# Performance work log

Measured on AMD Instinct MI355X. Metric: run time of the kernel, lower is better.

The kernel has to match this reference:

```python
import jax, jax.numpy as jnp
import numpy as np

D_MODEL = 2048
H_Q = 16
H_KV = 4
D_HEAD = D_MODEL // H_Q  # 128
G = H_Q // H_KV          # 4
B, S = 4, 2048


def setup_inputs() -> dict:
    key = jax.random.key(0)
    k1, k2, k3 = jax.random.split(key, 3)
    x = jax.random.normal(k1, (B, S, D_MODEL), dtype=jnp.float32)
    mask = jnp.zeros((S, S), dtype=jnp.float32)  # additive mask (zeros == no masking)
    # Linear weights, torch layout [out_features, in_features], bias=False
    Wqkv = jax.random.normal(k2, ((H_Q + 2 * H_KV) * D_HEAD, D_MODEL), dtype=jnp.float32) * (1.0 / np.sqrt(D_MODEL))
    Wo = jax.random.normal(k3, (D_MODEL, D_MODEL), dtype=jnp.float32) * (1.0 / np.sqrt(D_MODEL))
    return {"x": x, "mask": mask, "Wqkv": Wqkv, "Wo": Wo}


def reference(x, mask, Wqkv, Wo):
    d_q = H_Q * D_HEAD
    d_kv = H_KV * D_HEAD
    # fused QKV projection (Linear, no bias): x @ Wqkv.T
    qkv = jnp.einsum('bsd,ed->bse', x, Wqkv)  # [B,S,(H_Q+2*H_KV)*D_HEAD]
    q, k, v = jnp.split(qkv, [d_q, d_q + d_kv], axis=-1)
    q = q.reshape(B, S, H_Q, D_HEAD)
    k = k.reshape(B, S, H_KV, D_HEAD)
    v = v.reshape(B, S, H_KV, D_HEAD)
    # GQA: repeat_interleave KV heads G times along head axis
    k = jnp.repeat(k, G, axis=-2)  # [B,S,H_Q,D_HEAD]
    v = jnp.repeat(v, G, axis=-2)
    scale = 1.0 / np.sqrt(D_HEAD).astype(np.float32)
    scores = jnp.einsum('bqhd,bkhd->bhqk', q, k) * scale + mask  # [B,H_Q,S,S]
    attn = jax.nn.softmax(scores, axis=-1)
    out = jnp.einsum('bhqk,bkhd->bqhd', attn, v)  # [B,S,H_Q,D_HEAD]
    out = out.reshape(B, S, D_MODEL)
    return jnp.einsum('bsd,ed->bse', out, Wo)  # output projection
```

## Files before the change

kernel.cpp:

```cpp
#include <hip/hip_runtime.h>

#define D_MODEL 2048
#define S_LEN 2048
#define HQ 16
#define HKV 4
#define DH 128
#define QKV_W 3072
#define M_TOK 8192

typedef unsigned short u16;
typedef __bf16 bf16x8 __attribute__((ext_vector_type(8)));
typedef float f32x4 __attribute__((ext_vector_type(4)));
typedef float f32x16 __attribute__((ext_vector_type(16)));

__device__ __forceinline__ u16 f2bf(float f) {
  union { float f; unsigned u; } v; v.f = f;
  unsigned u = v.u;
  return (u16)((u + 0x7fffu + ((u >> 16) & 1u)) >> 16);
}

__device__ __forceinline__ bf16x8 ld_frag(const u16* p) {
  bf16x8 r; __builtin_memcpy(&r, p, 16); return r;
}

__device__ __forceinline__ void gl_lds16(const u16* g, u16* l) {
  __builtin_amdgcn_global_load_lds(
      (const __attribute__((address_space(1))) void*)g,
      (__attribute__((address_space(3))) void*)l, 16, 0, 0);
}

__device__ __forceinline__ unsigned cvtpk(float lo, float hi_) {
  unsigned r;
  asm("v_cvt_pk_bf16_f32 %0, %1, %2" : "=v"(r) : "v"(lo), "v"(hi_));
  return r;
}

#define MFMA(a, b, c) __builtin_amdgcn_mfma_f32_16x16x32_bf16(a, b, c, 0, 0, 0)
#define MFMA32(a, b, c) __builtin_amdgcn_mfma_f32_32x32x16_bf16(a, b, c, 0, 0, 0)

__device__ __forceinline__ float vmax16(const f32x16& v) {
  float a = fmaxf(fmaxf(v[0], v[1]), fmaxf(v[2], v[3]));
  float b = fmaxf(fmaxf(v[4], v[5]), fmaxf(v[6], v[7]));
  float c = fmaxf(fmaxf(v[8], v[9]), fmaxf(v[10], v[11]));
  float d = fmaxf(fmaxf(v[12], v[13]), fmaxf(v[14], v[15]));
  return fmaxf(fmaxf(a, b), fmaxf(c, d));
}
__device__ __forceinline__ float vsum16(const f32x16& v) {
  float a = (v[0] + v[1]) + (v[2] + v[3]);
  float b = (v[4] + v[5]) + (v[6] + v[7]);
  float c = (v[8] + v[9]) + (v[10] + v[11]);
  float d = (v[12] + v[13]) + (v[14] + v[15]);
  return (a + b) + (c + d);
}

__global__ __launch_bounds__(256) void k_f32_to_bf16(const float* __restrict__ s,
                                                     u16* __restrict__ d,
                                                     long scale_n) {
  long i = (long)(blockIdx.x * 256 + threadIdx.x) * 8;
  float sc = (i < scale_n) ? 0.08838834764831845f : 1.0f;
  float a[8];
  __builtin_memcpy(a, s + i, 32);
  u16 r[8];
#pragma unroll
  for (int j = 0; j < 8; ++j) r[j] = f2bf(a[j] * sc);
  __builtin_memcpy(d + i, r, 16);
}

template <int OUT_BF16>
__global__ __launch_bounds__(512, 2) void k_gemm256(const u16* __restrict__ A,
                                                    const u16* __restrict__ B,
                                                    void* __restrict__ C,
                                                    int M, int N, int K) {
  __shared__ u16 As[2][16384];
  __shared__ u16 Bs[2][16384];
  const int tid = threadIdx.x;
  const int lane = tid & 63;
  const int wid = tid >> 6;
  const int l15 = lane & 15, l4 = lane >> 4;
  const int wr = wid >> 2, wc = wid & 3;

  const int swz = (blockIdx.x & 7) * (gridDim.x >> 3) + (blockIdx.x >> 3);
  const int mt = M >> 8;
  const long tm = (long)(swz % mt) * 256;
  const long tn = (long)(swz / mt) * 256;

  const int cA = l4 ^ ((l15 >> 1) & 3);
  const int arow = wr * 128 + l15;
  const int brow = wc * 64 + l15;

  f32x4 acc[8][4] = {};
  bf16x8 af[4], bfr[4];

#define STG(dst, src, tbase, s, koff)                                      \
  do {                                                                     \
    _Pragma("unroll") for (int j = 0; j < 2; ++j) {                        \
      int p = tid + j * 512;                                               \
      int row = p >> 2, cc = p & 3;                                        \
      int g = cc ^ ((row >> 1) & 3);                                       \
      gl_lds16(src + (tbase + row) * (long)K + (koff) + (s) * 32 + g * 8,  \
               (dst) + (s) * 8192 + p * 8);                                \
    }                                                                      \
  } while (0)

#define DSR_A(ptr, s, mh)                                                  \
  _Pragma("unroll") for (int m = 0; m < 4; ++m)                            \
      af[m] = ld_frag((ptr) + (s) * 8192 + (arow + (mh) * 64 + m * 16) * 32 + cA * 8);
#define DSR_B(ptr, s)                                                      \
  _Pragma("unroll") for (int n = 0; n < 4; ++n)                            \
      bfr[n] = ld_frag((ptr) + (s) * 8192 + (brow + n * 16) * 32 + cA * 8);
#define MM(mh)                                                             \
  _Pragma("unroll") for (int m = 0; m < 4; ++m)                            \
      _Pragma("unroll") for (int n = 0; n < 4; ++n)                        \
          acc[(mh) * 4 + m][n] = MFMA(af[m], bfr[n], acc[(mh) * 4 + m][n]);
#define LGKM0                                              \
  asm volatile("s_waitcnt lgkmcnt(0)" ::: "memory");       \
  __builtin_amdgcn_sched_barrier(0)

  const int NT = K >> 6;
  STG(&As[0][0], A, tm, 0, 0);
  STG(&Bs[0][0], B, tn, 0, 0);
  STG(&As[0][0], A, tm, 1, 0);
  STG(&Bs[0][0], B, tn, 1, 0);

  for (int t = 0; t < NT; ++t) {
    const u16* as_ = &As[t & 1][0];
    const u16* bs_ = &Bs[t & 1][0];
    u16* an_ = &As[(t + 1) & 1][0];
    u16* bn_ = &Bs[(t + 1) & 1][0];
    const long kn = (long)(t + 1) * 64;
    const bool st = (t + 1 < NT);

    asm volatile("s_waitcnt vmcnt(4)" ::: "memory");
    __builtin_amdgcn_s_barrier();
    DSR_A(as_, 0, 0);
    DSR_B(bs_, 0);
    if (st) STG(an_, A, tm, 0, kn);
    LGKM0;
    __builtin_amdgcn_s_setprio(1); MM(0); __builtin_amdgcn_s_setprio(0);

    __builtin_amdgcn_s_barrier();
    DSR_A(as_, 0, 1);
    if (st) STG(bn_, B, tn, 0, kn);
    LGKM0;
    __builtin_amdgcn_s_setprio(1); MM(1); __builtin_amdgcn_s_setprio(0);

    if (st) {
      asm volatile("s_waitcnt vmcnt(4)" ::: "memory");
    } else {
      asm volatile("s_waitcnt vmcnt(0)" ::: "memory");
    }
    __builtin_amdgcn_s_barrier();
    DSR_A(as_, 1, 0);
    DSR_B(bs_, 1);
    if (st) STG(an_, A, tm, 1, kn);
    LGKM0;
    __builtin_amdgcn_s_setprio(1); MM(0); __builtin_amdgcn_s_setprio(0);

    __builtin_amdgcn_s_barrier();
    DSR_A(as_, 1, 1);
    if (st) STG(bn_, B, tn, 1, kn);
    LGKM0;
    __builtin_amdgcn_s_setprio(1); MM(1); __builtin_amdgcn_s_setprio(0);
  }
#undef STG
#undef DSR_A
#undef DSR_B
#undef MM
#undef LGKM0

#pragma unroll
  for (int m = 0; m < 8; ++m)
#pragma unroll
    for (int n = 0; n < 4; ++n)
#pragma unroll
      for (int i = 0; i < 4; ++i) {
        long row = tm + wr * 128 + m * 16 + l4 * 4 + i;
        long col = tn + wc * 64 + n * 16 + l15;
        if (OUT_BF16)
          ((u16*)C)[row * N + col] = f2bf(acc[m][n][i]);
        else
          ((float*)C)[row * N + col] = acc[m][n][i];
      }
}

__global__ __launch_bounds__(256) void k_vtrans(const u16* __restrict__ qkv,
                                                u16* __restrict__ vt) {
  __shared__ u16 T[64][68];
  const int tid = threadIdx.x;
  const int st = blockIdx.x;
  const int dt = blockIdx.y;
  const int bh = blockIdx.z;
  const int b = bh >> 2, kvh = bh & 3;
  const long s0 = (long)st * 64, d0 = (long)dt * 64;
#pragma unroll
  for (int j = 0; j < 2; ++j) {
    int chunk = tid + j * 256;
    int row = chunk >> 3, c8 = chunk & 7;
    u16 tmp[8];
    __builtin_memcpy(tmp,
                     qkv + ((long)b * S_LEN + s0 + row) * QKV_W + 2560 +
                         kvh * DH + d0 + c8 * 8,
                     16);
    __builtin_memcpy(&T[row][c8 * 8], tmp, 16);
  }
  __syncthreads();
#pragma unroll
  for (int j = 0; j < 2; ++j) {
    int chunk = tid + j * 256;
    int drow = chunk >> 3, c8 = chunk & 7;
    u16 tmp[8];
#pragma unroll
    for (int e = 0; e < 8; ++e) tmp[e] = T[c8 * 8 + e][drow];
    __builtin_memcpy(vt + ((long)bh * DH + d0 + drow) * S_LEN + s0 + c8 * 8,
                     tmp, 16);
  }
}

__global__ __launch_bounds__(512, 2) void k_attn(const u16* __restrict__ qkv,
                                                 const u16* __restrict__ vt,
                                                 u16* __restrict__ ao) {
  __shared__ u16 Ks[2][64 * 128];
  __shared__ u16 Vs[2][128 * 64];
  const int tid = threadIdx.x;
  const int lane = tid & 63;
  const int wid = tid >> 6;
  const int l31 = lane & 31, hi = lane >> 5;
  const int qt = blockIdx.x & 7;
  const int hh = (blockIdx.x >> 3) & 3;
  const int bkv = blockIdx.x >> 5;
  const int b = bkv >> 2, kvh = bkv & 3;
  const int h = kvh * 4 + hh;
  const long rowbase = (long)b * S_LEN;
  const int q0 = qt * 256 + wid * 32;
  const long vbase = (long)bkv * DH * S_LEN;

  bf16x8 qf[8];
  {
    const u16* qrow = qkv + (rowbase + q0 + l31) * QKV_W + h * DH;
#pragma unroll
    for (int kk = 0; kk < 8; ++kk) qf[kk] = ld_frag(qrow + kk * 16 + hi * 8);
  }

  f32x16 o[4] = {};
  float m_run = -3.0e38f, l_run = 0.f;

#define STAGE(buf, tile)                                                      \
  do {                                                                        \
    long s0_ = (long)(tile) * 64;                                             \
    _Pragma("unroll") for (int j = 0; j < 2; ++j) {                           \
      int chunk = (wid * 2 + j) * 64 + lane;                                  \
      int row = chunk >> 4, cc = chunk & 15;                                  \
      gl_lds16(qkv + (rowbase + s0_ + row) * QKV_W + 2048 + kvh * DH +        \
                   ((cc ^ (row & 7)) * 8),                                    \
               &Ks[buf][chunk * 8]);                                          \
    }                                                                         \
    _Pragma("unroll") for (int j = 0; j < 2; ++j) {                           \
      int chunk = (wid * 2 + j) * 64 + lane;                                  \
      int row = chunk >> 3, cc = chunk & 7;                                   \
      gl_lds16(vt + vbase + (long)row * S_LEN + s0_ + ((cc ^ (row & 7)) * 8), \
               &Vs[buf][chunk * 8]);                                          \
    }                                                                         \
  } while (0)

  STAGE(0, 0);
  __syncthreads();

  int cur = 0;
  for (int kt = 0; kt < 32; ++kt) {
    if (kt + 1 < 32) STAGE(cur ^ 1, kt + 1);

    f32x16 p0 = {}, p1 = {};
    {
      const u16* ks = &Ks[cur][0];
      __builtin_amdgcn_s_setprio(1);
#pragma unroll
      for (int kk = 0; kk < 8; ++kk) {
        int ch0 = ((2 * kk + hi) ^ (l31 & 7));
        int ch1 = ((2 * kk + hi) ^ ((l31 + 32) & 7));
        bf16x8 kf0 = ld_frag(ks + l31 * 128 + ch0 * 8);
        bf16x8 kf1 = ld_frag(ks + (32 + l31) * 128 + ch1 * 8);
        p0 = MFMA32(kf0, qf[kk], p0);
        p1 = MFMA32(kf1, qf[kk], p1);
      }
      __builtin_amdgcn_s_setprio(0);
    }

    float mx = fmaxf(vmax16(p0), vmax16(p1));
    mx = fmaxf(mx, __shfl_xor(mx, 32, 64));
    bool need = (mx > m_run + 8.0f);
    if (__any(need)) {
      float nm = fmaxf(m_run, mx);
      float alpha = __expf(m_run - nm);
      m_run = nm;
      l_run *= alpha;
#pragma unroll
      for (int n2 = 0; n2 < 4; ++n2)
#pragma unroll
        for (int r = 0; r < 16; ++r) o[n2][r] *= alpha;
    }
#pragma unroll
    for (int r = 0; r < 16; ++r) {
      p0[r] = __expf(p0[r] - m_run);
      p1[r] = __expf(p1[r] - m_run);
    }
    float ts = vsum16(p0) + vsum16(p1);
    ts += __shfl_xor(ts, 32, 64);
    l_run += ts;

    {
      const u16* vs = &Vs[cur][0];
      __builtin_amdgcn_s_setprio(1);
#pragma unroll
      for (int ks_ = 0; ks_ < 4; ++ks_) {
        const f32x16& pp = (ks_ < 2) ? p0 : p1;
        const int bb = 8 * (ks_ & 1);
        unsigned A0 = cvtpk(pp[bb + 0], pp[bb + 1]);
        unsigned A1 = cvtpk(pp[bb + 2], pp[bb + 3]);
        unsigned B0 = cvtpk(pp[bb + 4], pp[bb + 5]);
        unsigned B1 = cvtpk(pp[bb + 6], pp[bb + 7]);
        asm volatile("v_permlane32_swap_b32 %0, %1" : "+v"(A0), "+v"(B0));
        asm volatile("v_permlane32_swap_b32 %0, %1" : "+v"(A1), "+v"(B1));
        union { unsigned u[4]; bf16x8 v; } pu;
        pu.u[0] = A0; pu.u[1] = A1; pu.u[2] = B0; pu.u[3] = B1;
#pragma unroll
        for (int n2 = 0; n2 < 4; ++n2) {
          int vr = n2 * 32 + l31;
          int ch = ((2 * ks_ + hi) ^ (vr & 7));
          bf16x8 vf = ld_frag(vs + vr * 64 + ch * 8);
          o[n2] = MFMA32(vf, pu.v, o[n2]);
        }
      }
      __builtin_amdgcn_s_setprio(0);
    }
    __syncthreads();
    cur ^= 1;
  }

  {
    float inv = 1.0f / l_run;
    u16* orow = ao + (rowbase + q0 + l31) * D_MODEL + h * DH;
#pragma unroll
    for (int n2 = 0; n2 < 4; ++n2)
#pragma unroll
      for (int g = 0; g < 4; ++g) {
        u16 tmp[4];
#pragma unroll
        for (int e = 0; e < 4; ++e) tmp[e] = f2bf(o[n2][g * 4 + e] * inv);
        __builtin_memcpy(orow + n2 * 32 + g * 8 + 4 * hi, tmp, 8);
      }
  }
#undef STAGE
}

extern "C" void kernel_launch(void* const* d_in, const int* in_sizes, int n_in,
                              void* d_out, int out_size, void* d_ws,
                              size_t ws_size, hipStream_t stream) {
  const float* x = (const float*)d_in[0];
  const float* wqkv = (const float*)d_in[2];
  const float* wo = (const float*)d_in[3];
  char* ws = (char*)d_ws;
  u16* xb = (u16*)(ws);
  u16* wqkvb = (u16*)(ws + 33554432);
  u16* wob = (u16*)(ws + 46137344);
  u16* qkv = (u16*)(ws + 54525952);
  u16* vt = (u16*)(ws + 104857600);
  u16* ao = xb;

  k_f32_to_bf16<<<8192, 256, 0, stream>>>(x, xb, 0);
  k_f32_to_bf16<<<3072, 256, 0, stream>>>(wqkv, wqkvb, 4194304L);
  k_f32_to_bf16<<<2048, 256, 0, stream>>>(wo, wob, 0);
  k_gemm256<1><<<384, 512, 0, stream>>>(xb, wqkvb, qkv, M_TOK, QKV_W, D_MODEL);
  k_vtrans<<<dim3(32, 2, 16), 256, 0, stream>>>(qkv, vt);
  k_attn<<<512, 512, 0, stream>>>(qkv, vt, ao);
  k_gemm256<0><<<256, 512, 0, stream>>>(ao, wob, d_out, M_TOK, D_MODEL,
                                        D_MODEL);
}
```

Before: 397.3 us.

## Restructure GEMM mainloop into 4-stage LDS ring with 3-deep prefetch

The 256x256 GEMM mainloop changes from a double-buffered 64-wide K tile processed as two 32-wide halves to a 4-slot ring of 32-wide K tiles, with loads issued three tiles ahead. Each iteration now computes one 32-wide slice, and vmcnt waits are graded by how many stages are still in flight. The goal is to hide global-to-LDS latency behind more outstanding loads. In exchange it doubles the number of loop iterations and barriers per unit of K, and the barrier placement changes.

```diff
diff --git a/kernel.cpp b/kernel.cpp
--- a/kernel.cpp
+++ b/kernel.cpp
@@ -71,8 +71,8 @@
                                                     const u16* __restrict__ B,
                                                     void* __restrict__ C,
                                                     int M, int N, int K) {
-  __shared__ u16 As[2][16384];
-  __shared__ u16 Bs[2][16384];
+  __shared__ __attribute__((aligned(16))) u16 As[4][8192];
+  __shared__ __attribute__((aligned(16))) u16 Bs[4][8192];
   const int tid = threadIdx.x;
   const int lane = tid & 63;
   const int wid = tid >> 6;
@@ -91,76 +91,66 @@
   f32x4 acc[8][4] = {};
   bf16x8 af[4], bfr[4];
 
-#define STG(dst, src, tbase, s, koff)                                      \
-  do {                                                                     \
-    _Pragma("unroll") for (int j = 0; j < 2; ++j) {                        \
-      int p = tid + j * 512;                                               \
-      int row = p >> 2, cc = p & 3;                                        \
-      int g = cc ^ ((row >> 1) & 3);                                       \
-      gl_lds16(src + (tbase + row) * (long)K + (koff) + (s) * 32 + g * 8,  \
-               (dst) + (s) * 8192 + p * 8);                                \
-    }                                                                      \
+#define STG(dst, src, tbase, t_)                                          \
+  do {                                                                    \
+    _Pragma("unroll") for (int j = 0; j < 2; ++j) {                       \
+      int p = tid + j * 512;                                              \
+      int row = p >> 2, cc = p & 3;                                       \
+      int g = cc ^ ((row >> 1) & 3);                                      \
+      gl_lds16(src + (tbase + row) * (long)K + (long)(t_) * 32 + g * 8,   \
+               (dst) + p * 8);                                            \
+    }                                                                     \
   } while (0)
 
-#define DSR_A(ptr, s, mh)                                                  \
-  _Pragma("unroll") for (int m = 0; m < 4; ++m)                            \
-      af[m] = ld_frag((ptr) + (s) * 8192 + (arow + (mh) * 64 + m * 16) * 32 + cA * 8);
-#define DSR_B(ptr, s)                                                      \
-  _Pragma("unroll") for (int n = 0; n < 4; ++n)                            \
-      bfr[n] = ld_frag((ptr) + (s) * 8192 + (brow + n * 16) * 32 + cA * 8);
-#define MM(mh)                                                             \
-  _Pragma("unroll") for (int m = 0; m < 4; ++m)                            \
-      _Pragma("unroll") for (int n = 0; n < 4; ++n)                        \
+#define DSR_A(ptr, mh)                                                    \
+  _Pragma("unroll") for (int m = 0; m < 4; ++m)                           \
+      af[m] = ld_frag((ptr) + (arow + (mh) * 64 + m * 16) * 32 + cA * 8);
+#define DSR_B(ptr)                                                        \
+  _Pragma("unroll") for (int n = 0; n < 4; ++n)                           \
+      bfr[n] = ld_frag((ptr) + (brow + n * 16) * 32 + cA * 8);
+#define MM(mh)                                                            \
+  _Pragma("unroll") for (int m = 0; m < 4; ++m)                           \
+      _Pragma("unroll") for (int n = 0; n < 4; ++n)                       \
           acc[(mh) * 4 + m][n] = MFMA(af[m], bfr[n], acc[(mh) * 4 + m][n]);
 #define LGKM0                                              \
   asm volatile("s_waitcnt lgkmcnt(0)" ::: "memory");       \
   __builtin_amdgcn_sched_barrier(0)
 
-  const int NT = K >> 6;
-  STG(&As[0][0], A, tm, 0, 0);
-  STG(&Bs[0][0], B, tn, 0, 0);
-  STG(&As[0][0], A, tm, 1, 0);
-  STG(&Bs[0][0], B, tn, 1, 0);
+  const int NT = K >> 5;
+  STG(&As[0][0], A, tm, 0); STG(&Bs[0][0], B, tn, 0);
+  STG(&As[1][0], A, tm, 1); STG(&Bs[1][0], B, tn, 1);
+  STG(&As[2][0], A, tm, 2); STG(&Bs[2][0], B, tn, 2);
+  asm volatile("s_waitcnt vmcnt(8)" ::: "memory");
+  __builtin_amdgcn_s_barrier();
 
   for (int t = 0; t < NT; ++t) {
-    const u16* as_ = &As[t & 1][0];
-    const u16* bs_ = &Bs[t & 1][0];
-    u16* an_ = &As[(t + 1) & 1][0];
-    u16* bn_ = &Bs[(t + 1) & 1][0];
-    const long kn = (long)(t + 1) * 64;
-    const bool st = (t + 1 < NT);
-
-    asm volatile("s_waitcnt vmcnt(4)" ::: "memory");
+    const u16* as_ = &As[t & 3][0];
+    const u16* bs_ = &Bs[t & 3][0];
+    u16* an_ = &As[(t + 3) & 3][0];
+    u16* bn_ = &Bs[(t + 3) & 3][0];
+    const bool st = (t + 3 < NT);
+
+    DSR_A(as_, 0);
+    DSR_B(bs_);
+    if (st) STG(an_, A, tm, t + 3);
     __builtin_amdgcn_s_barrier();
-    DSR_A(as_, 0, 0);
-    DSR_B(bs_, 0);
-    if (st) STG(an_, A, tm, 0, kn);
     LGKM0;
     __builtin_amdgcn_s_setprio(1); MM(0); __builtin_amdgcn_s_setprio(0);
-
     __builtin_amdgcn_s_barrier();
-    DSR_A(as_, 0, 1);
-    if (st) STG(bn_, B, tn, 0, kn);
+
+    DSR_A(as_, 1);
+    if (st) STG(bn_, B, tn, t + 3);
+    __builtin_amdgcn_s_barrier();
     LGKM0;
     __builtin_amdgcn_s_setprio(1); MM(1); __builtin_amdgcn_s_setprio(0);
-
-    if (st) {
+    if (t + 3 < NT) {
+      asm volatile("s_waitcnt vmcnt(8)" ::: "memory");
+    } else if (t + 2 < NT) {
       asm volatile("s_waitcnt vmcnt(4)" ::: "memory");
-    } else {
+    } else if (t + 1 < NT) {
       asm volatile("s_waitcnt vmcnt(0)" ::: "memory");
     }
     __builtin_amdgcn_s_barrier();
-    DSR_A(as_, 1, 0);
-    DSR_B(bs_, 1);
-    if (st) STG(an_, A, tm, 1, kn);
-    LGKM0;
-    __builtin_amdgcn_s_setprio(1); MM(0); __builtin_amdgcn_s_setprio(0);
-
-    __builtin_amdgcn_s_barrier();
-    DSR_A(as_, 1, 1);
-    if (st) STG(bn_, B, tn, 1, kn);
-    LGKM0;
-    __builtin_amdgcn_s_setprio(1); MM(1); __builtin_amdgcn_s_setprio(0);
   }
 #undef STG
 #undef DSR_A
```

New measurement: 399.4 us. About the same (+0.5%).
